# Kernel tuning notes

Measured on AMD Instinct MI355X. Metric: run time of the kernel, lower is better.

The kernel has to match this reference:

```python
import jax, jax.numpy as jnp
import numpy as np

V, E, T, H, L, FF = 32000, 512, 2048, 8, 6, 2048
B = 2
HD = E // H
EPS = 1e-5


def setup_inputs() -> dict:
    key = jax.random.key(0)
    ks = iter(jax.random.split(key, 32))
    s = 0.02
    d = {
        "x": jax.random.randint(next(ks), (B, T), 0, V),
        "tok_emb": jax.random.normal(next(ks), (V, E), jnp.float32) * s,
        "pos_emb": jax.random.normal(next(ks), (T, E), jnp.float32) * s,
        "Wq": jax.random.normal(next(ks), (L, E, E), jnp.float32) * s,
        "bq": jnp.zeros((L, E), jnp.float32),
        "Wk": jax.random.normal(next(ks), (L, E, E), jnp.float32) * s,
        "bk": jnp.zeros((L, E), jnp.float32),
        "Wv": jax.random.normal(next(ks), (L, E, E), jnp.float32) * s,
        "bv": jnp.zeros((L, E), jnp.float32),
        "Wo": jax.random.normal(next(ks), (L, E, E), jnp.float32) * s,
        "bo": jnp.zeros((L, E), jnp.float32),
        "ln1_s": jnp.ones((L, E), jnp.float32),
        "ln1_b": jnp.zeros((L, E), jnp.float32),
        "ln2_s": jnp.ones((L, E), jnp.float32),
        "ln2_b": jnp.zeros((L, E), jnp.float32),
        "W1": jax.random.normal(next(ks), (L, E, FF), jnp.float32) * s,
        "b1": jnp.zeros((L, FF), jnp.float32),
        "W2": jax.random.normal(next(ks), (L, FF, E), jnp.float32) * s,
        "b2": jnp.zeros((L, E), jnp.float32),
        "Wout": jax.random.normal(next(ks), (E, V), jnp.float32) * s,
        "bout": jnp.zeros((V,), jnp.float32),
    }
    return d


def _layernorm(x, scale, bias):
    mu = jnp.mean(x, axis=-1, keepdims=True)
    var = jnp.var(x, axis=-1, keepdims=True)
    return (x - mu) * jax.lax.rsqrt(var + EPS) * scale + bias


def reference(x, tok_emb, pos_emb, Wq, bq, Wk, bk, Wv, bv, Wo, bo,
              ln1_s, ln1_b, ln2_s, ln2_b, W1, b1, W2, b2, Wout, bout):
    b, t = x.shape
    h = tok_emb[x] + pos_emb[:t][None]  # [b,t,E]
    causal = jnp.tril(jnp.ones((t, t), bool))  # True on/below diag
    for i in range(L):
        y = _layernorm(h, ln1_s[i], ln1_b[i])
        q = (y @ Wq[i] + bq[i]).reshape(b, t, H, HD)
        k = (y @ Wk[i] + bk[i]).reshape(b, t, H, HD)
        v = (y @ Wv[i] + bv[i]).reshape(b, t, H, HD)
        scores = jnp.einsum("bqhd,bkhd->bhqk", q, k) / np.sqrt(HD).astype(np.float32)
        scores = jnp.where(causal, scores, -jnp.inf)
        attn = jax.nn.softmax(scores, axis=-1)
        o = jnp.einsum("bhqk,bkhd->bqhd", attn, v).reshape(b, t, E)
        h = h + (o @ Wo[i] + bo[i])  # dropout is identity at eval
        y = _layernorm(h, ln2_s[i], ln2_b[i])
        ff = jax.nn.relu(y @ W1[i] + b1[i]) @ W2[i] + b2[i]
        h = h + ff
    return h @ Wout + bout  # [b,t,V]
```

## Files before the change

### kernel.cpp

```cpp
#include <hip/hip_runtime.h>
#include <cstdint>
#include <cstddef>

#define TOKENS 4096
#define E_ 512
#define T_ 2048
#define H_ 8
#define L_ 6
#define FF_ 2048
#define V_ 32000

typedef unsigned short u16;
typedef __attribute__((ext_vector_type(8))) short short8;
typedef __attribute__((ext_vector_type(4))) float f32x4;

__device__ __forceinline__ u16 f2b(float f) {
  union { float f; unsigned u; } x; x.f = f;
  unsigned r = x.u + 0x7fffu + ((x.u >> 16) & 1u);
  return (u16)(r >> 16);
}

__device__ __forceinline__ void gload_lds16(const void* g, void* l) {
  __builtin_amdgcn_global_load_lds((__attribute__((address_space(1))) void*)(uintptr_t)g,
                                   (__attribute__((address_space(3))) void*)l, 16, 0, 0);
}

template<int BF16OUT, int RESID, int RELU>
__global__ __launch_bounds__(256) void gemm_bt(
    const u16* __restrict__ A, const u16* __restrict__ BT,
    const float* __restrict__ bias, const float* __restrict__ resid,
    void* __restrict__ outp, int M, int N, int K, int ldc)
{
  __shared__ u16 a_sm[2][128 * 32];
  __shared__ u16 b_sm[2][128 * 32];
  const int tid  = threadIdx.x;
  const int wave = tid >> 6;
  const int lane = tid & 63;
  const int l16  = lane & 15;
  const int quad = lane >> 4;
  const int bm = blockIdx.y << 7;
  const int bn = blockIdx.x << 7;
  const int wr = (wave >> 1) << 6;
  const int wc = (wave & 1) << 6;

  const int srow = tid >> 2;
  const int soff = (tid & 3) << 3;
  const u16* ag0 = A  + (size_t)(bm + srow) * K + soff;
  const u16* ag1 = A  + (size_t)(bm + 64 + srow) * K + soff;
  const u16* bg0 = BT + (size_t)(bn + srow) * K + soff;
  const u16* bg1 = BT + (size_t)(bn + 64 + srow) * K + soff;

  auto stage = [&](int buf, int k0) {
    gload_lds16(ag0 + k0, a_sm[buf] + wave * 512);
    gload_lds16(ag1 + k0, a_sm[buf] + 2048 + wave * 512);
    gload_lds16(bg0 + k0, b_sm[buf] + wave * 512);
    gload_lds16(bg1 + k0, b_sm[buf] + 2048 + wave * 512);
  };

  f32x4 acc[4][4] = {};
  const int ksteps = K >> 5;
  stage(0, 0);
  int cur = 0;
  for (int t = 0; t < ksteps; ++t) {
    __syncthreads();
    if (t + 1 < ksteps) stage(cur ^ 1, (t + 1) << 5);
    short8 af[4], bf[4];
#pragma unroll
    for (int mt = 0; mt < 4; ++mt)
      af[mt] = *(const short8*)&a_sm[cur][(wr + mt * 16 + l16) * 32 + quad * 8];
#pragma unroll
    for (int nt = 0; nt < 4; ++nt)
      bf[nt] = *(const short8*)&b_sm[cur][(wc + nt * 16 + l16) * 32 + quad * 8];
#pragma unroll
    for (int mt = 0; mt < 4; ++mt)
#pragma unroll
      for (int nt = 0; nt < 4; ++nt)
        acc[mt][nt] = __builtin_amdgcn_mfma_f32_16x16x32_bf16(af[mt], bf[nt], acc[mt][nt], 0, 0, 0);
    cur ^= 1;
  }

#pragma unroll
  for (int mt = 0; mt < 4; ++mt) {
#pragma unroll
    for (int nt = 0; nt < 4; ++nt) {
      const int cg = bn + wc + nt * 16 + l16;
      const int rg = bm + wr + mt * 16 + quad * 4;
      const float bv = bias[cg];
#pragma unroll
      for (int i = 0; i < 4; ++i) {
        float v = acc[mt][nt][i] + bv;
        size_t idx = (size_t)(rg + i) * ldc + cg;
        if (RESID) v += resid[idx];
        if (RELU)  v = fmaxf(v, 0.f);
        if (BF16OUT) ((u16*)outp)[idx] = f2b(v);
        else         ((float*)outp)[idx] = v;
      }
    }
  }
}

template<int BF16OUT, int RELU>
__global__ __launch_bounds__(256) void gemm_bt64(
    const u16* __restrict__ A, const u16* __restrict__ BT,
    const float* __restrict__ bias, void* __restrict__ outp,
    int M, int N, int K, int ldc)
{
  __shared__ u16 a_sm[2][64 * 32];
  __shared__ u16 b_sm[2][128 * 32];
  const int tid  = threadIdx.x;
  const int wave = tid >> 6;
  const int lane = tid & 63;
  const int l16  = lane & 15;
  const int quad = lane >> 4;
  const int bm = blockIdx.y << 6;
  const int bn = blockIdx.x << 7;
  const int wr = (wave >> 1) << 5;
  const int wc = (wave & 1) << 6;

  const int srow = tid >> 2;
  const int soff = (tid & 3) << 3;
  const u16* ag  = A  + (size_t)(bm + srow) * K + soff;
  const u16* bg0 = BT + (size_t)(bn + srow) * K + soff;
  const u16* bg1 = BT + (size_t)(bn + 64 + srow) * K + soff;

  auto stage = [&](int buf, int k0) {
    gload_lds16(ag  + k0, a_sm[buf] + wave * 512);
    gload_lds16(bg0 + k0, b_sm[buf] + wave * 512);
    gload_lds16(bg1 + k0, b_sm[buf] + 2048 + wave * 512);
  };

  f32x4 acc[2][4] = {};
  const int ksteps = K >> 5;
  stage(0, 0);
  int cur = 0;
  for (int t = 0; t < ksteps; ++t) {
    __syncthreads();
    if (t + 1 < ksteps) stage(cur ^ 1, (t + 1) << 5);
    short8 af[2], bf[4];
#pragma unroll
    for (int mt = 0; mt < 2; ++mt)
      af[mt] = *(const short8*)&a_sm[cur][(wr + mt * 16 + l16) * 32 + quad * 8];
#pragma unroll
    for (int nt = 0; nt < 4; ++nt)
      bf[nt] = *(const short8*)&b_sm[cur][(wc + nt * 16 + l16) * 32 + quad * 8];
#pragma unroll
    for (int mt = 0; mt < 2; ++mt)
#pragma unroll
      for (int nt = 0; nt < 4; ++nt)
        acc[mt][nt] = __builtin_amdgcn_mfma_f32_16x16x32_bf16(af[mt], bf[nt], acc[mt][nt], 0, 0, 0);
    cur ^= 1;
  }

#pragma unroll
  for (int mt = 0; mt < 2; ++mt) {
#pragma unroll
    for (int nt = 0; nt < 4; ++nt) {
      const int cg = bn + wc + nt * 16 + l16;
      const int rg = bm + wr + mt * 16 + quad * 4;
      const float bv = bias[cg];
#pragma unroll
      for (int i = 0; i < 4; ++i) {
        float v = acc[mt][nt][i] + bv;
        size_t idx = (size_t)(rg + i) * ldc + cg;
        if (RELU)  v = fmaxf(v, 0.f);
        if (BF16OUT) ((u16*)outp)[idx] = f2b(v);
        else         ((float*)outp)[idx] = v;
      }
    }
  }
}

__global__ __launch_bounds__(256) void gemm_sk64(
    const u16* __restrict__ A, const u16* __restrict__ BT,
    float* __restrict__ part, int M, int N, int lda, int kLen)
{
  __shared__ u16 a_sm[2][64 * 32];
  __shared__ u16 b_sm[2][128 * 32];
  const int tid  = threadIdx.x;
  const int wave = tid >> 6;
  const int lane = tid & 63;
  const int l16  = lane & 15;
  const int quad = lane >> 4;
  const int bm = blockIdx.y << 6;
  const int bn = blockIdx.x << 7;
  const int wr = (wave >> 1) << 5;
  const int wc = (wave & 1) << 6;

  const u16* Ab = A  + (size_t)blockIdx.z * kLen;
  const u16* Bb = BT + (size_t)blockIdx.z * kLen;

  const int srow = tid >> 2;
  const int soff = (tid & 3) << 3;
  const u16* ag  = Ab + (size_t)(bm + srow) * lda + soff;
  const u16* bg0 = Bb + (size_t)(bn + srow) * lda + soff;
  const u16* bg1 = Bb + (size_t)(bn + 64 + srow) * lda + soff;

  auto stage = [&](int buf, int k0) {
    gload_lds16(ag  + k0, a_sm[buf] + wave * 512);
    gload_lds16(bg0 + k0, b_sm[buf] + wave * 512);
    gload_lds16(bg1 + k0, b_sm[buf] + 2048 + wave * 512);
  };

  f32x4 acc[2][4] = {};
  const int ksteps = kLen >> 5;
  stage(0, 0);
  int cur = 0;
  for (int t = 0; t < ksteps; ++t) {
    __syncthreads();
    if (t + 1 < ksteps) stage(cur ^ 1, (t + 1) << 5);
    short8 af[2], bf[4];
#pragma unroll
    for (int mt = 0; mt < 2; ++mt)
      af[mt] = *(const short8*)&a_sm[cur][(wr + mt * 16 + l16) * 32 + quad * 8];
#pragma unroll
    for (int nt = 0; nt < 4; ++nt)
      bf[nt] = *(const short8*)&b_sm[cur][(wc + nt * 16 + l16) * 32 + quad * 8];
#pragma unroll
    for (int mt = 0; mt < 2; ++mt)
#pragma unroll
      for (int nt = 0; nt < 4; ++nt)
        acc[mt][nt] = __builtin_amdgcn_mfma_f32_16x16x32_bf16(af[mt], bf[nt], acc[mt][nt], 0, 0, 0);
    cur ^= 1;
  }

  float* out = part + (size_t)blockIdx.z * M * N;
#pragma unroll
  for (int mt = 0; mt < 2; ++mt) {
#pragma unroll
    for (int nt = 0; nt < 4; ++nt) {
      const int cg = bn + wc + nt * 16 + l16;
      const int rg = bm + wr + mt * 16 + quad * 4;
#pragma unroll
      for (int i = 0; i < 4; ++i)
        out[(size_t)(rg + i) * N + cg] = acc[mt][nt][i];
    }
  }
}

__global__ __launch_bounds__(256) void attn_kernel(const u16* __restrict__ qkv,
                                                   u16* __restrict__ o)
{
  __shared__ u16 k_sm[2][64 * 64];
  __shared__ u16 vT_sm[2][64 * 64];
  __shared__ u16 p_sm[4 * 16 * 64];
  const int tid  = threadIdx.x;
  const int wave = tid >> 6;
  const int lane = tid & 63;
  const int l16  = lane & 15;
  const int quad = lane >> 4;
  const int j  = blockIdx.x;
  const int bh = blockIdx.y;
  const int b  = bh >> 3, h = bh & 7;
  const size_t base = (size_t)b * T_ * 1536;

  const int qrow = j * 64 + wave * 16 + l16;
  short8 aq[2];
#pragma unroll
  for (int half = 0; half < 2; ++half)
    aq[half] = *(const short8*)&qkv[base + (size_t)qrow * 1536 + h * 64 + half * 32 + quad * 8];

  f32x4 oacc[4] = {};
  float m_i[4] = {-INFINITY, -INFINITY, -INFINITY, -INFINITY};
  float l_i[4] = {0.f, 0.f, 0.f, 0.f};

  const int ksrc = ((tid & 7) ^ ((tid >> 3) & 7)) * 8;
  auto stageK = [&](int kt, int buf) {
    gload_lds16(qkv + base + (size_t)(kt * 64 + (tid >> 3)) * 1536 + 512 + h * 64 + ksrc,
                k_sm[buf] + wave * 512);
    gload_lds16(qkv + base + (size_t)(kt * 64 + 32 + (tid >> 3)) * 1536 + 512 + h * 64 + ksrc,
                k_sm[buf] + 2048 + wave * 512);
  };
  const int vt = tid >> 2, vd0 = (tid & 3) * 16;
  auto loadV = [&](int kt, short8* vr) {
    const u16* vp = &qkv[base + (size_t)(kt * 64 + vt) * 1536 + 1024 + h * 64 + vd0];
    vr[0] = *(const short8*)vp;
    vr[1] = *(const short8*)(vp + 8);
  };
  auto writeV = [&](int buf, const short8* vr) {
#pragma unroll
    for (int i = 0; i < 8; ++i) vT_sm[buf][(vd0 + i) * 64 + (vt ^ (i << 3))] = (u16)vr[0][i];
#pragma unroll
    for (int i = 0; i < 8; ++i) vT_sm[buf][(vd0 + 8 + i) * 64 + (vt ^ (i << 3))] = (u16)vr[1][i];
  };

  const int nkt = j + 1;
  short8 vr[2], vrn[2];
  stageK(0, 0);
  loadV(0, vr);
  writeV(0, vr);
  int cur = 0;
  for (int kt = 0; kt < nkt; ++kt) {
    __syncthreads();
    if (kt + 1 < nkt) { stageK(kt + 1, cur ^ 1); loadV(kt + 1, vrn); }

    f32x4 s[4] = {};
#pragma unroll
    for (int nt = 0; nt < 4; ++nt)
#pragma unroll
      for (int half = 0; half < 2; ++half) {
        short8 bk = *(const short8*)&k_sm[cur][(nt * 16 + l16) * 64 +
                                              (((half * 4 + quad) ^ (l16 & 7)) << 3)];
        s[nt] = __builtin_amdgcn_mfma_f32_16x16x32_bf16(aq[half], bk, s[nt], 0, 0, 0);
      }
#pragma unroll
    for (int nt = 0; nt < 4; ++nt)
#pragma unroll
      for (int i = 0; i < 4; ++i) {
        const int col = kt * 64 + nt * 16 + l16;
        const int row = j * 64 + wave * 16 + quad * 4 + i;
        float sv = s[nt][i] * 0.125f;
        s[nt][i] = (col <= row) ? sv : -INFINITY;
      }
    float rm[4], mn[4], alpha[4], rs[4], p[4][4];
#pragma unroll
    for (int i = 0; i < 4; ++i)
      rm[i] = fmaxf(fmaxf(s[0][i], s[1][i]), fmaxf(s[2][i], s[3][i]));
#pragma unroll
    for (int off = 1; off < 16; off <<= 1)
#pragma unroll
      for (int i = 0; i < 4; ++i) rm[i] = fmaxf(rm[i], __shfl_xor(rm[i], off));
#pragma unroll
    for (int i = 0; i < 4; ++i) {
      mn[i] = fmaxf(m_i[i], rm[i]);
      alpha[i] = __expf(m_i[i] - mn[i]);
      m_i[i] = mn[i];
#pragma unroll
      for (int nt = 0; nt < 4; ++nt) p[nt][i] = __expf(s[nt][i] - mn[i]);
      rs[i] = (p[0][i] + p[1][i]) + (p[2][i] + p[3][i]);
    }
#pragma unroll
    for (int off = 1; off < 16; off <<= 1)
#pragma unroll
      for (int i = 0; i < 4; ++i) rs[i] += __shfl_xor(rs[i], off);
#pragma unroll
    for (int i = 0; i < 4; ++i) l_i[i] = l_i[i] * alpha[i] + rs[i];
#pragma unroll
    for (int nt = 0; nt < 4; ++nt)
#pragma unroll
      for (int i = 0; i < 4; ++i) oacc[nt][i] *= alpha[i];
    u16* pw = p_sm + wave * 1024;
#pragma unroll
    for (int i = 0; i < 4; ++i) {
      const int pr = quad * 4 + i;
#pragma unroll
      for (int nt = 0; nt < 4; ++nt)
        pw[pr * 64 + ((nt * 16 + l16) ^ ((pr & 7) << 3))] = f2b(p[nt][i]);
    }
    asm volatile("s_waitcnt lgkmcnt(0)" ::: "memory");
    short8 pf[2];
#pragma unroll
    for (int kh = 0; kh < 2; ++kh)
      pf[kh] = *(const short8*)&pw[l16 * 64 + (((kh * 4 + quad) ^ (l16 & 7)) << 3)];
#pragma unroll
    for (int nt = 0; nt < 4; ++nt)
#pragma unroll
      for (int kh = 0; kh < 2; ++kh) {
        short8 bv = *(const short8*)&vT_sm[cur][(nt * 16 + l16) * 64 +
                                               (((kh * 4 + quad) ^ (l16 & 7)) << 3)];
        oacc[nt] = __builtin_amdgcn_mfma_f32_16x16x32_bf16(pf[kh], bv, oacc[nt], 0, 0, 0);
      }

    if (kt + 1 < nkt) writeV(cur ^ 1, vrn);
    cur ^= 1;
  }
#pragma unroll
  for (int nt = 0; nt < 4; ++nt)
#pragma unroll
    for (int i = 0; i < 4; ++i) {
      const int row = j * 64 + wave * 16 + quad * 4 + i;
      const float ov = oacc[nt][i] / l_i[i];
      o[(size_t)(b * T_ + row) * 512 + h * 64 + nt * 16 + l16] = f2b(ov);
    }
}

__device__ __forceinline__ void ln_emit(float2 hv, const float* __restrict__ sc,
                                        const float* __restrict__ bi, int tid,
                                        unsigned* __restrict__ yrow)
{
  float s = hv.x + hv.y;
  float q = hv.x * hv.x + hv.y * hv.y;
  for (int off = 32; off; off >>= 1) { s += __shfl_down(s, off); q += __shfl_down(q, off); }
  __shared__ float red[8];
  const int wave = tid >> 6, lane = tid & 63;
  if (!lane) { red[wave] = s; red[4 + wave] = q; }
  __syncthreads();
  if (tid == 0) {
    float ts = 0, tq = 0;
    for (int w = 0; w < 4; ++w) { ts += red[w]; tq += red[4 + w]; }
    red[0] = ts; red[4] = tq;
  }
  __syncthreads();
  const float mu = red[0] * (1.f / 512.f);
  const float var = red[4] * (1.f / 512.f) - mu * mu;
  const float rstd = rsqrtf(var + 1e-5f);
  const float y0 = (hv.x - mu) * rstd * sc[tid * 2]     + bi[tid * 2];
  const float y1 = (hv.y - mu) * rstd * sc[tid * 2 + 1] + bi[tid * 2 + 1];
  yrow[tid] = ((unsigned)f2b(y1) << 16) | (unsigned)f2b(y0);
}

template<int NS, int DOLN>
__global__ __launch_bounds__(256) void resid_ln_kernel(
    const float* __restrict__ part, const float* __restrict__ bias,
    float* __restrict__ h, const float* __restrict__ sc,
    const float* __restrict__ bi, u16* __restrict__ y)
{
  const int row = blockIdx.x, tid = threadIdx.x;
  float2 hv = ((const float2*)(h + (size_t)row * 512))[tid];
  const float2 bv = ((const float2*)bias)[tid];
#pragma unroll
  for (int s = 0; s < NS; ++s) {
    const float2 pv = ((const float2*)(part + ((size_t)s * TOKENS + row) * 512))[tid];
    hv.x += pv.x; hv.y += pv.y;
  }
  hv.x += bv.x; hv.y += bv.y;
  ((float2*)(h + (size_t)row * 512))[tid] = hv;
  if (DOLN)
    ln_emit(hv, sc, bi, tid, (unsigned*)(y + (size_t)row * 512));
  else
    ((unsigned*)y)[(size_t)row * 256 + tid] = ((unsigned)f2b(hv.y) << 16) | (unsigned)f2b(hv.x);
}

__global__ __launch_bounds__(256) void embed_ln_kernel(const int* __restrict__ x,
                                                       const float* __restrict__ tok,
                                                       const float* __restrict__ pos,
                                                       const float* __restrict__ sc,
                                                       const float* __restrict__ bi,
                                                       float* __restrict__ h,
                                                       u16* __restrict__ y)
{
  const int row = blockIdx.x, tid = threadIdx.x;
  const int t = row & (T_ - 1);
  const int tk = x[row];
  const float2 a = ((const float2*)tok)[(size_t)tk * 256 + tid];
  const float2 p = ((const float2*)pos)[(size_t)t * 256 + tid];
  float2 hv = make_float2(a.x + p.x, a.y + p.y);
  ((float2*)(h + (size_t)row * 512))[tid] = hv;
  ln_emit(hv, sc, bi, tid, (unsigned*)(y + (size_t)row * 512));
}

__global__ void transW(const float* __restrict__ src, u16* __restrict__ dst,
                       int K, int N, long sStr, long dStr)
{
  __shared__ float tile[32][33];
  const int l = blockIdx.z;
  const float* S = src + (size_t)l * sStr;
  u16* D = dst + (size_t)l * dStr;
  const int n0 = blockIdx.x * 32, k0 = blockIdx.y * 32;
  const int tx = threadIdx.x, ty = threadIdx.y;
#pragma unroll
  for (int i = 0; i < 4; ++i)
    tile[ty + 8 * i][tx] = S[(size_t)(k0 + ty + 8 * i) * N + n0 + tx];
  __syncthreads();
#pragma unroll
  for (int i = 0; i < 4; ++i)
    D[(size_t)(n0 + ty + 8 * i) * K + k0 + tx] = f2b(tile[tx][ty + 8 * i]);
}

__global__ __launch_bounds__(256) void bias_cat_kernel(const float* __restrict__ bq,
                                                       const float* __restrict__ bk,
                                                       const float* __restrict__ bv,
                                                       float* __restrict__ o)
{
  const int i = blockIdx.x * 256 + threadIdx.x;
  if (i >= L_ * 1536) return;
  const int l = i / 1536, c = i % 1536;
  float v = (c < 512) ? bq[l * 512 + c] : (c < 1024) ? bk[l * 512 + c - 512] : bv[l * 512 + c - 1024];
  o[i] = v;
}

extern "C" void kernel_launch(void* const* d_in, const int* in_sizes, int n_in,
                              void* d_out, int out_size, void* d_ws, size_t ws_size,
                              hipStream_t stream) {
  const int*   x     = (const int*)d_in[0];
  const float* tok   = (const float*)d_in[1];
  const float* pos   = (const float*)d_in[2];
  const float* Wq    = (const float*)d_in[3];
  const float* bq    = (const float*)d_in[4];
  const float* Wk    = (const float*)d_in[5];
  const float* bk    = (const float*)d_in[6];
  const float* Wv    = (const float*)d_in[7];
  const float* bv    = (const float*)d_in[8];
  const float* Wo    = (const float*)d_in[9];
  const float* bo    = (const float*)d_in[10];
  const float* ln1s  = (const float*)d_in[11];
  const float* ln1b  = (const float*)d_in[12];
  const float* ln2s  = (const float*)d_in[13];
  const float* ln2b  = (const float*)d_in[14];
  const float* W1    = (const float*)d_in[15];
  const float* b1    = (const float*)d_in[16];
  const float* W2    = (const float*)d_in[17];
  const float* b2    = (const float*)d_in[18];
  const float* Wout  = (const float*)d_in[19];
  const float* bout  = (const float*)d_in[20];

  char* ws = (char*)d_ws;
  size_t off = 0;
  auto alloc = [&](size_t bytes) { char* p = ws + off; off += (bytes + 255) & ~(size_t)255; return p; };
  u16*   qkvT  = (u16*)alloc((size_t)L_ * 1536 * 512 * 2);
  u16*   WoT   = (u16*)alloc((size_t)L_ * 512 * 512 * 2);
  u16*   W1T   = (u16*)alloc((size_t)L_ * 2048 * 512 * 2);
  u16*   W2T   = (u16*)alloc((size_t)L_ * 512 * 2048 * 2);
  u16*   WoutT = (u16*)alloc((size_t)V_ * 512 * 2);
  float* bqkv  = (float*)alloc((size_t)L_ * 1536 * 4);
  float* h     = (float*)alloc((size_t)TOKENS * 512 * 4);
  u16*   y     = (u16*)alloc((size_t)TOKENS * 512 * 2);
  u16*   qkv   = (u16*)alloc((size_t)TOKENS * 1536 * 2);
  u16*   obuf  = (u16*)alloc((size_t)TOKENS * 512 * 2);
  u16*   ff    = (u16*)alloc((size_t)TOKENS * 2048 * 2);
  u16*   hb    = (u16*)alloc((size_t)TOKENS * 512 * 2);
  float* part  = (float*)alloc((size_t)4 * TOKENS * 512 * 4);
  (void)ws_size; (void)in_sizes; (void)n_in; (void)out_size;

  transW<<<dim3(16, 16, L_), dim3(32, 8), 0, stream>>>(Wq, qkvT,             512, 512, 512L * 512, 1536L * 512);
  transW<<<dim3(16, 16, L_), dim3(32, 8), 0, stream>>>(Wk, qkvT + 512 * 512, 512, 512, 512L * 512, 1536L * 512);
  transW<<<dim3(16, 16, L_), dim3(32, 8), 0, stream>>>(Wv, qkvT + 1024 * 512,512, 512, 512L * 512, 1536L * 512);
  transW<<<dim3(16, 16, L_), dim3(32, 8), 0, stream>>>(Wo, WoT,              512, 512, 512L * 512, 512L * 512);
  transW<<<dim3(64, 16, L_), dim3(32, 8), 0, stream>>>(W1, W1T,  512, 2048, 512L * 2048, 2048L * 512);
  transW<<<dim3(16, 64, L_), dim3(32, 8), 0, stream>>>(W2, W2T, 2048,  512, 2048L * 512, 512L * 2048);
  transW<<<dim3(1000, 16, 1), dim3(32, 8), 0, stream>>>(Wout, WoutT, 512, V_, 0, 0);
  bias_cat_kernel<<<36, 256, 0, stream>>>(bq, bk, bv, bqkv);

  embed_ln_kernel<<<TOKENS, 256, 0, stream>>>(x, tok, pos, ln1s, ln1b, h, y);

  for (int l = 0; l < L_; ++l) {
    gemm_bt64<1, 0><<<dim3(12, 64), 256, 0, stream>>>(
        y, qkvT + (size_t)l * 1536 * 512, bqkv + l * 1536, qkv, TOKENS, 1536, 512, 1536);
    attn_kernel<<<dim3(32, 16), 256, 0, stream>>>(qkv, obuf);
    gemm_sk64<<<dim3(4, 64, 2), 256, 0, stream>>>(
        obuf, WoT + (size_t)l * 512 * 512, part, TOKENS, 512, 512, 256);
    resid_ln_kernel<2, 1><<<TOKENS, 256, 0, stream>>>(
        part, bo + l * 512, h, ln2s + l * 512, ln2b + l * 512, y);
    gemm_bt64<1, 1><<<dim3(16, 64), 256, 0, stream>>>(
        y, W1T + (size_t)l * 2048 * 512, b1 + l * 2048, ff, TOKENS, 2048, 512, 2048);
    gemm_sk64<<<dim3(4, 64, 2), 256, 0, stream>>>(
        ff, W2T + (size_t)l * 512 * 2048, part, TOKENS, 512, 2048, 1024);
    if (l < L_ - 1)
      resid_ln_kernel<2, 1><<<TOKENS, 256, 0, stream>>>(
          part, b2 + l * 512, h, ln1s + (l + 1) * 512, ln1b + (l + 1) * 512, y);
    else
      resid_ln_kernel<2, 0><<<TOKENS, 256, 0, stream>>>(
          part, b2 + l * 512, h, nullptr, nullptr, hb);
  }

  gemm_bt<0, 0, 0><<<dim3(250, 32), 256, 0, stream>>>(
      hb, WoutT, bout, nullptr, (float*)d_out, TOKENS, V_, 512, V_);
}
```

Before: 1.833 ms.

## Fuse split-K reduction with residual and layernorm via last-block atomic counter

The split-K projection GEMMs now use a per-row-tile atomic counter. The last finishing block sums the partials, adds bias and the residual, and emits the layernormed bf16 activations, so the separate resid_ln kernel launches go away. The weight transposes and bias concatenation are merged into one transpose launch plus the embed kernel. Attention reverses its query-tile order for the second batch to balance causal work across blocks. The cost is a threadfence/atomic tail and a 64-row reduction handled by a single block per tile, with one row per 4 threads and large register arrays.

```diff
diff --git a/kernel.cpp b/kernel.cpp
--- a/kernel.cpp
+++ b/kernel.cpp
@@ -170,9 +170,13 @@
   }
 }
 
-__global__ __launch_bounds__(256) void gemm_sk64(
+template<int DOLN, int Z>
+__global__ __launch_bounds__(256) void gemm_skr64(
     const u16* __restrict__ A, const u16* __restrict__ BT,
-    float* __restrict__ part, int M, int N, int lda, int kLen)
+    float* __restrict__ part, int* __restrict__ cnt,
+    const float* __restrict__ bias, float* __restrict__ h,
+    const float* __restrict__ sc, const float* __restrict__ bi,
+    u16* __restrict__ yout, int lda, int kLen)
 {
   __shared__ u16 a_sm[2][64 * 32];
   __shared__ u16 b_sm[2][128 * 32];
@@ -223,7 +227,7 @@
     cur ^= 1;
   }
 
-  float* out = part + (size_t)blockIdx.z * M * N;
+  float* out = part + (size_t)blockIdx.z * (TOKENS * 512);
 #pragma unroll
   for (int mt = 0; mt < 2; ++mt) {
 #pragma unroll
@@ -232,8 +236,68 @@
       const int rg = bm + wr + mt * 16 + quad * 4;
 #pragma unroll
       for (int i = 0; i < 4; ++i)
-        out[(size_t)(rg + i) * N + cg] = acc[mt][nt][i];
-    }
+        out[(size_t)(rg + i) * 512 + cg] = acc[mt][nt][i];
+    }
+  }
+  __threadfence();
+
+  __shared__ int isLast;
+  if (tid == 0) {
+    const int old = atomicAdd(&cnt[blockIdx.y], 1);
+    const int last = (old == (int)(gridDim.x * gridDim.z) - 1);
+    if (last) atomicExch(&cnt[blockIdx.y], 0);
+    isLast = last;
+  }
+  __syncthreads();
+  if (!isLast) return;
+  __threadfence();
+
+  const int r  = bm + (tid >> 2);
+  const int c4 = (tid & 3) << 2;
+  float4 v[32];
+#pragma unroll
+  for (int i = 0; i < 32; ++i) {
+    const int col = i * 16 + c4;
+    float4 a = *(const float4*)&h[(size_t)r * 512 + col];
+    const float4 b = *(const float4*)&bias[col];
+    a.x += b.x; a.y += b.y; a.z += b.z; a.w += b.w;
+#pragma unroll
+    for (int z = 0; z < Z; ++z) {
+      const float4 p = *(const float4*)&part[((size_t)z * TOKENS + r) * 512 + col];
+      a.x += p.x; a.y += p.y; a.z += p.z; a.w += p.w;
+    }
+    *(float4*)&h[(size_t)r * 512 + col] = a;
+    v[i] = a;
+  }
+  float s = 0.f, q = 0.f;
+#pragma unroll
+  for (int i = 0; i < 32; ++i) {
+    s += (v[i].x + v[i].y) + (v[i].z + v[i].w);
+    q += (v[i].x * v[i].x + v[i].y * v[i].y) + (v[i].z * v[i].z + v[i].w * v[i].w);
+  }
+  s += __shfl_xor(s, 1); s += __shfl_xor(s, 2);
+  q += __shfl_xor(q, 1); q += __shfl_xor(q, 2);
+  const float mu = s * (1.f / 512.f);
+  const float var = q * (1.f / 512.f) - mu * mu;
+  const float rstd = rsqrtf(var + 1e-5f);
+#pragma unroll
+  for (int i = 0; i < 32; ++i) {
+    const int col = i * 16 + c4;
+    float y0, y1, y2, y3;
+    if (DOLN) {
+      const float4 s4 = *(const float4*)&sc[col];
+      const float4 b4 = *(const float4*)&bi[col];
+      y0 = (v[i].x - mu) * rstd * s4.x + b4.x;
+      y1 = (v[i].y - mu) * rstd * s4.y + b4.y;
+      y2 = (v[i].z - mu) * rstd * s4.z + b4.z;
+      y3 = (v[i].w - mu) * rstd * s4.w + b4.w;
+    } else {
+      y0 = v[i].x; y1 = v[i].y; y2 = v[i].z; y3 = v[i].w;
+    }
+    uint2 pk;
+    pk.x = ((unsigned)f2b(y1) << 16) | (unsigned)f2b(y0);
+    pk.y = ((unsigned)f2b(y3) << 16) | (unsigned)f2b(y2);
+    *(uint2*)(yout + (size_t)r * 512 + col) = pk;
   }
 }
 
@@ -248,8 +312,8 @@
   const int lane = tid & 63;
   const int l16  = lane & 15;
   const int quad = lane >> 4;
-  const int j  = blockIdx.x;
   const int bh = blockIdx.y;
+  const int j  = (bh < 8) ? blockIdx.x : 31 - blockIdx.x;
   const int b  = bh >> 3, h = bh & 7;
   const size_t base = (size_t)b * T_ * 1536;
 
@@ -398,37 +462,29 @@
   yrow[tid] = ((unsigned)f2b(y1) << 16) | (unsigned)f2b(y0);
 }
 
-template<int NS, int DOLN>
-__global__ __launch_bounds__(256) void resid_ln_kernel(
-    const float* __restrict__ part, const float* __restrict__ bias,
-    float* __restrict__ h, const float* __restrict__ sc,
-    const float* __restrict__ bi, u16* __restrict__ y)
-{
-  const int row = blockIdx.x, tid = threadIdx.x;
-  float2 hv = ((const float2*)(h + (size_t)row * 512))[tid];
-  const float2 bv = ((const float2*)bias)[tid];
-#pragma unroll
-  for (int s = 0; s < NS; ++s) {
-    const float2 pv = ((const float2*)(part + ((size_t)s * TOKENS + row) * 512))[tid];
-    hv.x += pv.x; hv.y += pv.y;
-  }
-  hv.x += bv.x; hv.y += bv.y;
-  ((float2*)(h + (size_t)row * 512))[tid] = hv;
-  if (DOLN)
-    ln_emit(hv, sc, bi, tid, (unsigned*)(y + (size_t)row * 512));
-  else
-    ((unsigned*)y)[(size_t)row * 256 + tid] = ((unsigned)f2b(hv.y) << 16) | (unsigned)f2b(hv.x);
-}
-
 __global__ __launch_bounds__(256) void embed_ln_kernel(const int* __restrict__ x,
                                                        const float* __restrict__ tok,
                                                        const float* __restrict__ pos,
                                                        const float* __restrict__ sc,
                                                        const float* __restrict__ bi,
+                                                       const float* __restrict__ bq,
+                                                       const float* __restrict__ bk,
+                                                       const float* __restrict__ bv,
+                                                       float* __restrict__ bqkv,
+                                                       int* __restrict__ cnt,
                                                        float* __restrict__ h,
                                                        u16* __restrict__ y)
 {
   const int row = blockIdx.x, tid = threadIdx.x;
+  if (row == 0 && tid < 64) cnt[tid] = 0;
+  if (row < 36) {
+    const int i = row * 256 + tid;
+    if (i < L_ * 1536) {
+      const int l = i / 1536, c = i % 1536;
+      bqkv[i] = (c < 512) ? bq[l * 512 + c]
+              : (c < 1024) ? bk[l * 512 + c - 512] : bv[l * 512 + c - 1024];
+    }
+  }
   const int t = row & (T_ - 1);
   const int tk = x[row];
   const float2 a = ((const float2*)tok)[(size_t)tk * 256 + tid];
@@ -438,14 +494,42 @@
   ln_emit(hv, sc, bi, tid, (unsigned*)(y + (size_t)row * 512));
 }
 
-__global__ void transW(const float* __restrict__ src, u16* __restrict__ dst,
-                       int K, int N, long sStr, long dStr)
+__global__ void transW_all(const float* __restrict__ Wq, const float* __restrict__ Wk,
+                           const float* __restrict__ Wv, const float* __restrict__ Wo,
+                           const float* __restrict__ W1, const float* __restrict__ W2,
+                           const float* __restrict__ Wout,
+                           u16* __restrict__ qkvT, u16* __restrict__ WoT,
+                           u16* __restrict__ W1T, u16* __restrict__ W2T,
+                           u16* __restrict__ WoutT)
 {
   __shared__ float tile[32][33];
-  const int l = blockIdx.z;
-  const float* S = src + (size_t)l * sStr;
-  u16* D = dst + (size_t)l * dStr;
-  const int n0 = blockIdx.x * 32, k0 = blockIdx.y * 32;
+  int f = blockIdx.x;
+  const float* S; u16* D; int N, Kd, n0, k0;
+  if (f < 16000) {
+    S = Wout; D = WoutT; N = 32000; Kd = 512;
+    n0 = (f % 1000) * 32; k0 = (f / 1000) * 32;
+  } else {
+    f -= 16000;
+    const int l = f / 3072, r = f % 3072;
+    if (r < 1024) {
+      const int w = r >> 8, rr = r & 255;
+      S = (w == 0 ? Wq : w == 1 ? Wk : w == 2 ? Wv : Wo) + (size_t)l * 512 * 512;
+      D = (w < 3) ? qkvT + (size_t)l * 1536 * 512 + (size_t)w * 512 * 512
+                  : WoT + (size_t)l * 512 * 512;
+      N = 512; Kd = 512;
+      n0 = (rr & 15) * 32; k0 = (rr >> 4) * 32;
+    } else if (r < 2048) {
+      const int rr = r - 1024;
+      S = W1 + (size_t)l * 512 * 2048; D = W1T + (size_t)l * 2048 * 512;
+      N = 2048; Kd = 512;
+      n0 = (rr & 63) * 32; k0 = (rr >> 6) * 32;
+    } else {
+      const int rr = r - 2048;
+      S = W2 + (size_t)l * 2048 * 512; D = W2T + (size_t)l * 512 * 2048;
+      N = 512; Kd = 2048;
+      n0 = (rr & 15) * 32; k0 = (rr >> 4) * 32;
+    }
+  }
   const int tx = threadIdx.x, ty = threadIdx.y;
 #pragma unroll
   for (int i = 0; i < 4; ++i)
@@ -453,19 +537,7 @@
   __syncthreads();
 #pragma unroll
   for (int i = 0; i < 4; ++i)
-    D[(size_t)(n0 + ty + 8 * i) * K + k0 + tx] = f2b(tile[tx][ty + 8 * i]);
-}
-
-__global__ __launch_bounds__(256) void bias_cat_kernel(const float* __restrict__ bq,
-                                                       const float* __restrict__ bk,
-                                                       const float* __restrict__ bv,
-                                                       float* __restrict__ o)
-{
-  const int i = blockIdx.x * 256 + threadIdx.x;
-  if (i >= L_ * 1536) return;
-  const int l = i / 1536, c = i % 1536;
-  float v = (c < 512) ? bq[l * 512 + c] : (c < 1024) ? bk[l * 512 + c - 512] : bv[l * 512 + c - 1024];
-  o[i] = v;
+    D[(size_t)(n0 + ty + 8 * i) * Kd + k0 + tx] = f2b(tile[tx][ty + 8 * i]);
 }
 
 extern "C" void kernel_launch(void* const* d_in, const int* in_sizes, int n_in,
@@ -509,37 +581,32 @@
   u16*   ff    = (u16*)alloc((size_t)TOKENS * 2048 * 2);
   u16*   hb    = (u16*)alloc((size_t)TOKENS * 512 * 2);
   float* part  = (float*)alloc((size_t)4 * TOKENS * 512 * 4);
+  int*   cnt   = (int*)alloc(64 * sizeof(int));
   (void)ws_size; (void)in_sizes; (void)n_in; (void)out_size;
 
-  transW<<<dim3(16, 16, L_), dim3(32, 8), 0, stream>>>(Wq, qkvT,             512, 512, 512L * 512, 1536L * 512);
-  transW<<<dim3(16, 16, L_), dim3(32, 8), 0, stream>>>(Wk, qkvT + 512 * 512, 512, 512, 512L * 512, 1536L * 512);
-  transW<<<dim3(16, 16, L_), dim3(32, 8), 0, stream>>>(Wv, qkvT + 1024 * 512,512, 512, 512L * 512, 1536L * 512);
-  transW<<<dim3(16, 16, L_), dim3(32, 8), 0, stream>>>(Wo, WoT,              512, 512, 512L * 512, 512L * 512);
-  transW<<<dim3(64, 16, L_), dim3(32, 8), 0, stream>>>(W1, W1T,  512, 2048, 512L * 2048, 2048L * 512);
-  transW<<<dim3(16, 64, L_), dim3(32, 8), 0, stream>>>(W2, W2T, 2048,  512, 2048L * 512, 512L * 2048);
-  transW<<<dim3(1000, 16, 1), dim3(32, 8), 0, stream>>>(Wout, WoutT, 512, V_, 0, 0);
-  bias_cat_kernel<<<36, 256, 0, stream>>>(bq, bk, bv, bqkv);
-
-  embed_ln_kernel<<<TOKENS, 256, 0, stream>>>(x, tok, pos, ln1s, ln1b, h, y);
+  transW_all<<<34432, dim3(32, 8), 0, stream>>>(Wq, Wk, Wv, Wo, W1, W2, Wout,
+                                                qkvT, WoT, W1T, W2T, WoutT);
+
+  embed_ln_kernel<<<TOKENS, 256, 0, stream>>>(x, tok, pos, ln1s, ln1b,
+                                              bq, bk, bv, bqkv, cnt, h, y);
 
   for (int l = 0; l < L_; ++l) {
     gemm_bt64<1, 0><<<dim3(12, 64), 256, 0, stream>>>(
         y, qkvT + (size_t)l * 1536 * 512, bqkv + l * 1536, qkv, TOKENS, 1536, 512, 1536);
     attn_kernel<<<dim3(32, 16), 256, 0, stream>>>(qkv, obuf);
-    gemm_sk64<<<dim3(4, 64, 2), 256, 0, stream>>>(
-        obuf, WoT + (size_t)l * 512 * 512, part, TOKENS, 512, 512, 256);
-    resid_ln_kernel<2, 1><<<TOKENS, 256, 0, stream>>>(
-        part, bo + l * 512, h, ln2s + l * 512, ln2b + l * 512, y);
+    gemm_skr64<1, 2><<<dim3(4, 64, 2), 256, 0, stream>>>(
+        obuf, WoT + (size_t)l * 512 * 512, part, cnt, bo + l * 512, h,
+        ln2s + l * 512, ln2b + l * 512, y, 512, 256);
     gemm_bt64<1, 1><<<dim3(16, 64), 256, 0, stream>>>(
         y, W1T + (size_t)l * 2048 * 512, b1 + l * 2048, ff, TOKENS, 2048, 512, 2048);
-    gemm_sk64<<<dim3(4, 64, 2), 256, 0, stream>>>(
-        ff, W2T + (size_t)l * 512 * 2048, part, TOKENS, 512, 2048, 1024);
     if (l < L_ - 1)
-      resid_ln_kernel<2, 1><<<TOKENS, 256, 0, stream>>>(
-          part, b2 + l * 512, h, ln1s + (l + 1) * 512, ln1b + (l + 1) * 512, y);
+      gemm_skr64<1, 2><<<dim3(4, 64, 2), 256, 0, stream>>>(
+          ff, W2T + (size_t)l * 512 * 2048, part, cnt, b2 + l * 512, h,
+          ln1s + (l + 1) * 512, ln1b + (l + 1) * 512, y, 2048, 1024);
     else
-      resid_ln_kernel<2, 0><<<TOKENS, 256, 0, stream>>>(
-          part, b2 + l * 512, h, nullptr, nullptr, hb);
+      gemm_skr64<0, 2><<<dim3(4, 64, 2), 256, 0, stream>>>(
+          ff, W2T + (size_t)l * 512 * 2048, part, cnt, b2 + l * 512, h,
+          nullptr, nullptr, hb, 2048, 1024);
   }
 
   gemm_bt<0, 0, 0><<<dim3(250, 32), 256, 0, stream>>>(
```

New measurement: 2.671 ms. 1.46x slower.
